# Kernel tuning notes

Hardware: AMD Instinct MI355X
Metric: run time of the kernel (lower is better)

Reference implementation:

```python
import jax, jax.numpy as jnp
import numpy as np

NEG = -9e15  # mask value used by dense GAT-style implementations
ALPHA = 0.1  # leaky_relu negative slope (init arg)
DENSITY = 0.05  # sparsity of the incidence/adjacency operator


def setup_inputs() -> dict:
    key = jax.random.key(0)
    ks = jax.random.split(key, 7)
    n_s, n_t = 8192, 4096
    s_in = t_in = 128
    s_out = t_out = 64
    H = 4
    input1 = jax.random.normal(ks[0], (n_s, s_in), dtype=jnp.float32)
    input2 = jax.random.normal(ks[1], (n_t, t_in), dtype=jnp.float32)
    A_opt = (jax.random.uniform(ks[2], (n_t, n_s)) < DENSITY).astype(jnp.float32)
    # per-head params, stacked on leading head axis (math identical to num_heads separate layers)
    Ws = jax.random.normal(ks[3], (H, s_in, t_out), dtype=jnp.float32) * (1.0 / np.sqrt(s_in))
    Wt = jax.random.normal(ks[4], (H, t_in, s_out), dtype=jnp.float32) * (1.0 / np.sqrt(t_in))
    a_src = jax.random.normal(ks[5], (H, t_out), dtype=jnp.float32) * 0.1
    a_tgt = jax.random.normal(ks[6], (H, s_out), dtype=jnp.float32) * 0.1
    return {"input1": input1, "input2": input2, "A_opt": A_opt,
            "Ws": Ws, "Wt": Wt, "a_src": a_src, "a_tgt": a_tgt}


def _forward(input1, input2, A_opt, Ws, Wt, a_src, a_tgt):
    # hs: source feats projected to target_out space; ht: target feats -> source_out space
    hs = jnp.einsum('si,hio->hso', input1, Ws)          # [H, n_s, t_out]
    ht = jnp.einsum('ti,hio->hto', input2, Wt)          # [H, n_t, s_out]
    # additive GAT score, broadcast over the [n_t, n_s] grid
    e = jax.nn.leaky_relu(
        jnp.einsum('hto,ho->ht', ht, a_tgt)[:, :, None]
        + jnp.einsum('hso,ho->hs', hs, a_src)[:, None, :],
        negative_slope=ALPHA)                            # [H, n_t, n_s]
    mask = (A_opt != 0.0)[None]                          # [1, n_t, n_s]
    e_masked = jnp.where(mask, e, NEG)
    attn_ts = jax.nn.softmax(e_masked, axis=-1)          # normalize over source cells
    attn_st = jax.nn.softmax(e_masked, axis=-2)          # normalize over target cells
    h_ts = jax.nn.elu(jnp.einsum('hts,hso->hto', attn_ts, hs))  # [H, n_t, t_out]
    h_st = jax.nn.elu(jnp.einsum('hts,hto->hso', attn_st, ht))  # [H, n_s, s_out]
    # concatenate heads along feature dim (concatenate=True)
    out_st = jnp.transpose(h_st, (1, 0, 2)).reshape(input1.shape[0], -1)  # [n_s, H*s_out]
    out_ts = jnp.transpose(h_ts, (1, 0, 2)).reshape(input2.shape[0], -1)  # [n_t, H*t_out]
    return out_st, out_ts


def reference(input1, input2, A_opt, Ws, Wt, a_src, a_tgt):
    return _forward(input1, input2, A_opt, Ws, Wt, a_src, a_tgt)
```

## Files before the change

### kernel.cpp

```cpp
#include <hip/hip_runtime.h>
#include <hip/hip_bf16.h>

#define H 4
#define NS 8192
#define NT 4096
#define DIN 128
#define DOUT 64
#define ROW_CAP 1024
#define COL_CAP 512
#define NEGBIG -3.0e38f

typedef unsigned short ushort8_t __attribute__((ext_vector_type(8)));

__device__ __forceinline__ float lrelu(float x) { return x >= 0.f ? x : 0.1f * x; }
__device__ __forceinline__ float eluf(float x) { return x > 0.f ? x : expm1f(x); }

__device__ __forceinline__ float waveMax(float v) {
    for (int off = 32; off > 0; off >>= 1) v = fmaxf(v, __shfl_xor(v, off, 64));
    return v;
}
__device__ __forceinline__ float waveSum(float v) {
    for (int off = 32; off > 0; off >>= 1) v += __shfl_xor(v, off, 64);
    return v;
}
__device__ __forceinline__ float rlane(float v, int l) {
    return __int_as_float(__builtin_amdgcn_readlane(__float_as_int(v), l));
}

__global__ __launch_bounds__(256) void proj_kernel(
    const float* __restrict__ X, const float* __restrict__ W,
    const float* __restrict__ a_vec, float* __restrict__ Hout,
    float* __restrict__ b_out, int N) {
    __shared__ float w_lds[DIN * DOUT];
    __shared__ float a_lds[16 * 129];
    const int h = blockIdx.y;
    const int row0 = blockIdx.x * 16;
    const int tid = threadIdx.x;

    const float* Wh = W + (size_t)h * DIN * DOUT;
    for (int i = tid; i < DIN * DOUT; i += 256) w_lds[i] = Wh[i];
    for (int i = tid; i < 16 * DIN; i += 256) {
        int r = i >> 7, c = i & 127;
        a_lds[r * 129 + c] = X[(size_t)(row0 + r) * DIN + c];
    }
    __syncthreads();

    const int fg = (tid & 15) * 4;
    const int r = tid >> 4;
    const float* ar = &a_lds[r * 129];
    float acc0 = 0.f, acc1 = 0.f, acc2 = 0.f, acc3 = 0.f;
#pragma unroll 8
    for (int i = 0; i < DIN; ++i) {
        float av = ar[i];
        float4 wv = *reinterpret_cast<const float4*>(&w_lds[i * DOUT + fg]);
        acc0 += av * wv.x; acc1 += av * wv.y; acc2 += av * wv.z; acc3 += av * wv.w;
    }
    const int s = row0 + r;
    float4 o = make_float4(acc0, acc1, acc2, acc3);
    *reinterpret_cast<float4*>(&Hout[((size_t)h * N + s) * DOUT + fg]) = o;

    const float* av = a_vec + h * DOUT + fg;
    float part = acc0 * av[0] + acc1 * av[1] + acc2 * av[2] + acc3 * av[3];
    for (int off = 8; off > 0; off >>= 1) part += __shfl_xor(part, off, 64);
    if ((tid & 15) == 0) b_out[(size_t)h * N + s] = part;
}

__global__ __launch_bounds__(256) void mask_kernel(
    const float* __restrict__ A,
    unsigned long long* __restrict__ mask_row,
    unsigned long long* __restrict__ mask_col) {
    __shared__ unsigned long long rowbits[64];
    const int s0 = blockIdx.x * 64;
    const int t0 = blockIdx.y * 64;
    const int lane = threadIdx.x & 63;
    const int w = threadIdx.x >> 6;
    for (int rr = w; rr < 64; rr += 4) {
        const int t = t0 + rr;
        float v = A[(size_t)t * NS + s0 + lane];
        unsigned long long word = __ballot(v != 0.0f);
        if (lane == 0) {
            mask_row[(size_t)t * (NS / 64) + (s0 >> 6)] = word;
            rowbits[rr] = word;
        }
    }
    __syncthreads();
    if (threadIdx.x < 64) {
        const int j = threadIdx.x;
        unsigned long long cw = 0;
        for (int rr = 0; rr < 64; ++rr) cw |= ((rowbits[rr] >> j) & 1ull) << rr;
        mask_col[(size_t)(s0 + j) * (NT / 64) + (t0 >> 6)] = cw;
    }
}

template <int NW, int CAP>
__device__ __forceinline__ int compact_list(
    const unsigned long long* __restrict__ mask, size_t mask_row_off,
    unsigned short* list, int* wtot, int tid) {
    unsigned long long word = 0;
    int c = 0;
    if (tid < NW) {
        word = mask[mask_row_off + tid];
        c = __popcll(word);
    }
    int incl = c;
#pragma unroll
    for (int d = 1; d < 64; d <<= 1) {
        int v = __shfl_up(incl, d, 64);
        if ((tid & 63) >= d) incl += v;
    }
    if ((tid & 63) == 63) wtot[tid >> 6] = incl;
    __syncthreads();
    int base_off = 0;
#pragma unroll
    for (int wv = 0; wv < (NW / 64); ++wv) {
        int v = wtot[wv];
        if (wv < (tid >> 6)) base_off += v;
    }
    int nnz = 0;
#pragma unroll
    for (int wv = 0; wv < (NW / 64); ++wv) nnz += wtot[wv];
    if (tid < NW) {
        int off = base_off + incl - c;
        unsigned long long wd = word;
        const int base = tid * 64;
        while (wd) {
            int b = __ffsll((long long)wd) - 1;
            if (off < CAP) list[off] = (unsigned short)(base + b);
            ++off;
            wd &= wd - 1;
        }
    }
    nnz = nnz > CAP ? CAP : nnz;
    int nk64 = (nnz + 63) & ~63;
    for (int j = nnz + tid; j < nk64; j += 256) list[j] = 0;
    return nnz;
}

template <int KMAX>
__device__ __forceinline__ float attn_core(
    const unsigned short* __restrict__ list, int nnz,
    const float* __restrict__ bvec,
    float bias,
    const float* __restrict__ src,
    int lane) {
    const int nk = (nnz + 63) >> 6;
    float wreg[KMAX];

    float m = NEGBIG;
#pragma unroll
    for (int k = 0; k < KMAX; ++k) {
        if (k >= nk) break;
        int j = (k << 6) + lane;
        float p = NEGBIG;
        if (j < nnz) p = bvec[list[j]];
        wreg[k] = p;
        m = fmaxf(m, p);
    }
    m = waveMax(m);
    const float mrow = lrelu(bias + m);

    float ssum = 0.f;
#pragma unroll
    for (int k = 0; k < KMAX; ++k) {
        if (k >= nk) break;
        int j = (k << 6) + lane;
        float w = 0.f;
        if (j < nnz) w = __expf(lrelu(bias + wreg[k]) - mrow);
        wreg[k] = w;
        ssum += w;
    }
    ssum = waveSum(ssum);
    const float rs = ssum > 0.f ? 1.0f / ssum : 0.f;

    const char* basec = (const char*)src;
    const unsigned laneByte = (unsigned)lane << 2;
    float a0 = 0.f, a1 = 0.f, a2 = 0.f, a3 = 0.f;
    float a4 = 0.f, a5 = 0.f, a6 = 0.f, a7 = 0.f;
#pragma unroll
    for (int k = 0; k < KMAX; ++k) {
        if (k >= nk) break;
        const float wk = wreg[k];
        const ushort8_t* lp = reinterpret_cast<const ushort8_t*>(&list[k << 6]);
        for (int g = 0; g < 8; ++g) {
            ushort8_t ix = lp[g];
            const int l = g << 3;
            a0 += rlane(wk, l + 0) * *(const float*)(basec + (((unsigned)ix[0]) << 8) + laneByte);
            a1 += rlane(wk, l + 1) * *(const float*)(basec + (((unsigned)ix[1]) << 8) + laneByte);
            a2 += rlane(wk, l + 2) * *(const float*)(basec + (((unsigned)ix[2]) << 8) + laneByte);
            a3 += rlane(wk, l + 3) * *(const float*)(basec + (((unsigned)ix[3]) << 8) + laneByte);
            a4 += rlane(wk, l + 4) * *(const float*)(basec + (((unsigned)ix[4]) << 8) + laneByte);
            a5 += rlane(wk, l + 5) * *(const float*)(basec + (((unsigned)ix[5]) << 8) + laneByte);
            a6 += rlane(wk, l + 6) * *(const float*)(basec + (((unsigned)ix[6]) << 8) + laneByte);
            a7 += rlane(wk, l + 7) * *(const float*)(basec + (((unsigned)ix[7]) << 8) + laneByte);
        }
    }
    float acc = ((a0 + a1) + (a2 + a3)) + ((a4 + a5) + (a6 + a7));
    return acc * rs;
}

__global__ __launch_bounds__(256) void attn_row_kernel(
    const unsigned long long* __restrict__ mask_row,
    const float* __restrict__ bs, const float* __restrict__ bt,
    const float* __restrict__ hs, float* __restrict__ out_ts) {
    __shared__ __align__(16) unsigned short list[ROW_CAP];
    __shared__ int wtot[4];

    const int t = blockIdx.x;
    const int tid = threadIdx.x;
    const int nnz = compact_list<NS / 64, ROW_CAP>(
        mask_row, (size_t)t * (NS / 64), list, wtot, tid);
    __syncthreads();

    const int h = tid >> 6, lane = tid & 63;
    const float btv = bt[(size_t)h * NT + t];
    float r = attn_core<ROW_CAP / 64>(list, nnz, bs + (size_t)h * NS, btv,
                                      hs + (size_t)h * NS * DOUT, lane);
    out_ts[(size_t)t * (H * DOUT) + h * DOUT + lane] = eluf(r);
}

__global__ __launch_bounds__(256) void attn_col_kernel(
    const unsigned long long* __restrict__ mask_col,
    const float* __restrict__ bs, const float* __restrict__ bt,
    const float* __restrict__ ht, float* __restrict__ out_st) {
    __shared__ __align__(16) unsigned short list[COL_CAP];
    __shared__ int wtot[4];

    const int s = blockIdx.x;
    const int tid = threadIdx.x;
    const int nnz = compact_list<NT / 64, COL_CAP>(
        mask_col, (size_t)s * (NT / 64), list, wtot, tid);
    __syncthreads();

    const int h = tid >> 6, lane = tid & 63;
    const float bsv = bs[(size_t)h * NS + s];
    float r = attn_core<COL_CAP / 64>(list, nnz, bt + (size_t)h * NT, bsv,
                                      ht + (size_t)h * NT * DOUT, lane);
    out_st[(size_t)s * (H * DOUT) + h * DOUT + lane] = eluf(r);
}

extern "C" void kernel_launch(void* const* d_in, const int* in_sizes, int n_in,
                              void* d_out, int out_size, void* d_ws, size_t ws_size,
                              hipStream_t stream) {
    const float* input1 = (const float*)d_in[0];
    const float* input2 = (const float*)d_in[1];
    const float* A      = (const float*)d_in[2];
    const float* Ws     = (const float*)d_in[3];
    const float* Wt     = (const float*)d_in[4];
    const float* a_src  = (const float*)d_in[5];
    const float* a_tgt  = (const float*)d_in[6];
    float* out = (float*)d_out;

    char* ws = (char*)d_ws;
    float* hs = (float*)(ws + 0);
    float* ht = (float*)(ws + 8388608);
    float* bs = (float*)(ws + 12582912);
    float* bt = (float*)(ws + 12713984);
    unsigned long long* mask_row = (unsigned long long*)(ws + 12779520);
    unsigned long long* mask_col = (unsigned long long*)(ws + 16973824);

    proj_kernel<<<dim3(NS / 16, H), 256, 0, stream>>>(input1, Ws, a_src, hs, bs, NS);
    proj_kernel<<<dim3(NT / 16, H), 256, 0, stream>>>(input2, Wt, a_tgt, ht, bt, NT);
    mask_kernel<<<dim3(NS / 64, NT / 64), 256, 0, stream>>>(A, mask_row, mask_col);
    attn_row_kernel<<<NT, 256, 0, stream>>>(mask_row, bs, bt, hs,
                                            out + (size_t)NS * (H * DOUT));
    attn_col_kernel<<<NS, 256, 0, stream>>>(mask_col, bs, bt, ht, out);
}
```

Baseline: 460.2 us.

## Assign one row per wave with per-wave compaction and head-grouped block mapping

Each wave now handles its own target/source row for a single head: it compacts the mask row into a per-wave list using an in-wave prefix scan, so the block-wide barrier and shared wave totals go away. Blocks are remapped so the four waves of a block share one head across four rows, which keeps the gathered hs/ht slice for that head hot in cache. The trade-off is that the mask compaction is repeated once per head (four times per row), and the per-wave serial scan loops over more words.

```diff
diff --git a/kernel.cpp b/kernel.cpp
--- a/kernel.cpp
+++ b/kernel.cpp
@@ -92,47 +92,34 @@
     }
 }
 
-template <int NW, int CAP>
-__device__ __forceinline__ int compact_list(
-    const unsigned long long* __restrict__ mask, size_t mask_row_off,
-    unsigned short* list, int* wtot, int tid) {
-    unsigned long long word = 0;
-    int c = 0;
-    if (tid < NW) {
-        word = mask[mask_row_off + tid];
-        c = __popcll(word);
-    }
-    int incl = c;
-#pragma unroll
-    for (int d = 1; d < 64; d <<= 1) {
-        int v = __shfl_up(incl, d, 64);
-        if ((tid & 63) >= d) incl += v;
-    }
-    if ((tid & 63) == 63) wtot[tid >> 6] = incl;
-    __syncthreads();
-    int base_off = 0;
-#pragma unroll
-    for (int wv = 0; wv < (NW / 64); ++wv) {
-        int v = wtot[wv];
-        if (wv < (tid >> 6)) base_off += v;
-    }
-    int nnz = 0;
-#pragma unroll
-    for (int wv = 0; wv < (NW / 64); ++wv) nnz += wtot[wv];
-    if (tid < NW) {
-        int off = base_off + incl - c;
-        unsigned long long wd = word;
-        const int base = tid * 64;
+template <int NWORDS, int CAP>
+__device__ __forceinline__ int wave_compact(
+    const unsigned long long* __restrict__ mask, size_t word_base,
+    unsigned short* list, int lane) {
+    int total = 0;
+#pragma unroll
+    for (int c = 0; c < NWORDS / 64; ++c) {
+        unsigned long long wd = mask[word_base + c * 64 + lane];
+        int cnt = __popcll(wd);
+        int incl = cnt;
+#pragma unroll
+        for (int d = 1; d < 64; d <<= 1) {
+            int v = __shfl_up(incl, d, 64);
+            if (lane >= d) incl += v;
+        }
+        int off = total + incl - cnt;
+        const int base = (c * 64 + lane) * 64;
         while (wd) {
             int b = __ffsll((long long)wd) - 1;
             if (off < CAP) list[off] = (unsigned short)(base + b);
             ++off;
             wd &= wd - 1;
         }
-    }
-    nnz = nnz > CAP ? CAP : nnz;
+        total += __shfl(incl, 63, 64);
+    }
+    int nnz = total > CAP ? CAP : total;
     int nk64 = (nnz + 63) & ~63;
-    for (int j = nnz + tid; j < nk64; j += 256) list[j] = 0;
+    for (int j = nnz + lane; j < nk64; j += 64) list[j] = 0;
     return nnz;
 }
 
@@ -202,18 +189,19 @@
     const unsigned long long* __restrict__ mask_row,
     const float* __restrict__ bs, const float* __restrict__ bt,
     const float* __restrict__ hs, float* __restrict__ out_ts) {
-    __shared__ __align__(16) unsigned short list[ROW_CAP];
-    __shared__ int wtot[4];
-
-    const int t = blockIdx.x;
-    const int tid = threadIdx.x;
-    const int nnz = compact_list<NS / 64, ROW_CAP>(
-        mask_row, (size_t)t * (NS / 64), list, wtot, tid);
-    __syncthreads();
-
-    const int h = tid >> 6, lane = tid & 63;
+    __shared__ __align__(16) unsigned short list[4][ROW_CAP];
+
+    const int bid = blockIdx.x;
+    const int w = threadIdx.x >> 6, lane = threadIdx.x & 63;
+    const int h = (bid & 7) >> 1;
+    const int tgroup = ((bid >> 3) << 1) | (bid & 1);
+    const int t = tgroup * 4 + w;
+
+    const int nnz = wave_compact<NS / 64, ROW_CAP>(
+        mask_row, (size_t)t * (NS / 64), list[w], lane);
+
     const float btv = bt[(size_t)h * NT + t];
-    float r = attn_core<ROW_CAP / 64>(list, nnz, bs + (size_t)h * NS, btv,
+    float r = attn_core<ROW_CAP / 64>(list[w], nnz, bs + (size_t)h * NS, btv,
                                       hs + (size_t)h * NS * DOUT, lane);
     out_ts[(size_t)t * (H * DOUT) + h * DOUT + lane] = eluf(r);
 }
@@ -222,18 +210,19 @@
     const unsigned long long* __restrict__ mask_col,
     const float* __restrict__ bs, const float* __restrict__ bt,
     const float* __restrict__ ht, float* __restrict__ out_st) {
-    __shared__ __align__(16) unsigned short list[COL_CAP];
-    __shared__ int wtot[4];
-
-    const int s = blockIdx.x;
-    const int tid = threadIdx.x;
-    const int nnz = compact_list<NT / 64, COL_CAP>(
-        mask_col, (size_t)s * (NT / 64), list, wtot, tid);
-    __syncthreads();
-
-    const int h = tid >> 6, lane = tid & 63;
+    __shared__ __align__(16) unsigned short list[4][COL_CAP];
+
+    const int bid = blockIdx.x;
+    const int w = threadIdx.x >> 6, lane = threadIdx.x & 63;
+    const int h = (bid & 7) >> 1;
+    const int sgroup = ((bid >> 3) << 1) | (bid & 1);
+    const int s = sgroup * 4 + w;
+
+    const int nnz = wave_compact<NT / 64, COL_CAP>(
+        mask_col, (size_t)s * (NT / 64), list[w], lane);
+
     const float bsv = bs[(size_t)h * NS + s];
-    float r = attn_core<COL_CAP / 64>(list, nnz, bt + (size_t)h * NT, bsv,
+    float r = attn_core<COL_CAP / 64>(list[w], nnz, bt + (size_t)h * NT, bsv,
                                       ht + (size_t)h * NT * DOUT, lane);
     out_st[(size_t)s * (H * DOUT) + h * DOUT + lane] = eluf(r);
 }
@@ -261,7 +250,7 @@
     proj_kernel<<<dim3(NS / 16, H), 256, 0, stream>>>(input1, Ws, a_src, hs, bs, NS);
     proj_kernel<<<dim3(NT / 16, H), 256, 0, stream>>>(input2, Wt, a_tgt, ht, bt, NT);
     mask_kernel<<<dim3(NS / 64, NT / 64), 256, 0, stream>>>(A, mask_row, mask_col);
-    attn_row_kernel<<<NT, 256, 0, stream>>>(mask_row, bs, bt, hs,
-                                            out + (size_t)NS * (H * DOUT));
-    attn_col_kernel<<<NS, 256, 0, stream>>>(mask_col, bs, bt, ht, out);
-}
+    attn_row_kernel<<<NT * H / 4, 256, 0, stream>>>(mask_row, bs, bt, hs,
+                                                    out + (size_t)NS * (H * DOUT));
+    attn_col_kernel<<<NS * H / 4, 256, 0, stream>>>(mask_col, bs, bt, ht, out);
+}
```

Measured after the change: 428.4 us. -6.9%, faster.
